# Kernel tuning notes

Hardware: AMD Instinct MI355X
Metric: run time of the kernel (lower is better)

Reference implementation:

```python
import jax, jax.numpy as jnp
import numpy as np

N_NODES = 100000
N_EDGES = 3200000
N_FEAT = 128
HIDDEN = 16
N_CLASSES = 10
N_GRAPHS = 512


def setup_inputs() -> dict:
    key = jax.random.key(0)
    ks = jax.random.split(key, 12)
    x = jax.random.normal(ks[0], (N_NODES, N_FEAT), dtype=jnp.float32)
    edge_index = jax.random.randint(ks[1], (2, N_EDGES), 0, N_NODES, dtype=jnp.int64)
    batch = jnp.sort(jax.random.randint(ks[2], (N_NODES,), 0, N_GRAPHS, dtype=jnp.int64))
    def glorot(k, fan_in, fan_out):
        s = jnp.sqrt(6.0 / (fan_in + fan_out)).astype(jnp.float32)
        return jax.random.uniform(k, (fan_in, fan_out), jnp.float32, -s, s)
    W1 = glorot(ks[3], N_FEAT, HIDDEN); b1 = jnp.zeros((HIDDEN,), jnp.float32)
    W2 = glorot(ks[4], HIDDEN, HIDDEN); b2 = jnp.zeros((HIDDEN,), jnp.float32)
    W3 = glorot(ks[5], HIDDEN, HIDDEN); b3 = jnp.zeros((HIDDEN,), jnp.float32)
    Wlin = glorot(ks[6], HIDDEN, N_CLASSES)
    blin = jnp.zeros((N_CLASSES,), jnp.float32)
    return {"x": x, "edge_index": edge_index, "batch": batch,
            "W1": W1, "b1": b1, "W2": W2, "b2": b2, "W3": W3, "b3": b3,
            "Wlin": Wlin, "blin": blin}


def _gcn_conv(x, W, b, src, dst, norm, n):
    # h = X W ; out[dst] += norm * h[src] ; + bias
    h = x @ W
    out = jax.ops.segment_sum(h[src] * norm[:, None], dst, num_segments=n)
    return out + b


def reference(x, edge_index, batch, W1, b1, W2, b2, W3, b3, Wlin, blin):
    n = x.shape[0]
    loop = jnp.arange(n, dtype=edge_index.dtype)
    src = jnp.concatenate([edge_index[0], loop])  # add self-loops (PyG GCNConv default)
    dst = jnp.concatenate([edge_index[1], loop])
    # symmetric degree normalization: deg over destination (incl. self-loops)
    deg = jax.ops.segment_sum(jnp.ones_like(dst, dtype=x.dtype), dst, num_segments=n)
    dinv = jnp.where(deg > 0, jax.lax.rsqrt(jnp.maximum(deg, 1.0)), 0.0)
    norm = dinv[src] * dinv[dst]  # [E+N]

    h = jax.nn.relu(_gcn_conv(x, W1, b1, src, dst, norm, n))
    h = jax.nn.relu(_gcn_conv(h, W2, b2, src, dst, norm, n))
    h = _gcn_conv(h, W3, b3, src, dst, norm, n)
    # global add pool over graphs
    pooled = jax.ops.segment_sum(h, batch, num_segments=N_GRAPHS)  # [G, hidden]
    # dropout p=0.5 is identity in eval mode
    return pooled @ Wlin + blin
```

## Files before the change

### kernel.cpp

```cpp
#include <hip/hip_runtime.h>
#include <hip/hip_fp16.h>

#define N_NODES   100000
#define N_EDGES   3200000
#define N_FEAT    128
#define HIDDEN    16
#define N_CLASSES 10
#define N_GRAPHS  512
#define NPB       256
#define NBUCKET   391
#define SLACK     9216
#define EPT       16


__global__ void cursor_init_kernel(int* __restrict__ cur) {
    int i = blockIdx.x * 256 + threadIdx.x;
    if (i < NBUCKET) cur[i] = i * SLACK;
}

__global__ void partition_kernel(const int* __restrict__ src, const int* __restrict__ dst,
                                 int* __restrict__ cur, unsigned* __restrict__ part) {
    __shared__ int cnt[NBUCKET];
    __shared__ int rk[NBUCKET];
    __shared__ int base[NBUCKET];
    int tid = threadIdx.x;
    for (int i = tid; i < NBUCKET; i += 256) { cnt[i] = 0; rk[i] = 0; }
    __syncthreads();
    int s0 = blockIdx.x * (256 * EPT);
#pragma unroll
    for (int i = 0; i < EPT; ++i) {
        int e = s0 + i * 256 + tid;
        if (e < N_EDGES) atomicAdd(&cnt[dst[e] >> 8], 1);
    }
    __syncthreads();
    for (int i = tid; i < NBUCKET; i += 256) {
        int c = cnt[i];
        base[i] = c ? atomicAdd(&cur[i], c) : 0;
    }
    __syncthreads();
#pragma unroll
    for (int i = 0; i < EPT; ++i) {
        int e = s0 + i * 256 + tid;
        if (e < N_EDGES) {
            int d = dst[e];
            int b = d >> 8;
            int r = atomicAdd(&rk[b], 1);
            part[base[b] + r] = (unsigned)src[e] | ((unsigned)(d & 255) << 17);
        }
    }
}

__global__ void build_csr_kernel(const unsigned* __restrict__ part, const int* __restrict__ cur,
                                 int* __restrict__ rp_beg, int* __restrict__ rp_end,
                                 float* __restrict__ dinv, int* __restrict__ csr) {
    __shared__ int ncnt[256];
    __shared__ int s[256];
    int b   = blockIdx.x;
    int tid = threadIdx.x;
    int beg = b * SLACK, end = cur[b];
    ncnt[tid] = 0;
    __syncthreads();
    for (int j = beg + tid; j < end; j += 256)
        atomicAdd(&ncnt[(part[j] >> 17) & 255], 1);
    __syncthreads();
    int deg = ncnt[tid];
    s[tid] = deg;
    __syncthreads();
    for (int off = 1; off < 256; off <<= 1) {
        int t = (tid >= off) ? s[tid - off] : 0;
        __syncthreads();
        s[tid] += t;
        __syncthreads();
    }
    int excl = s[tid] - deg;
    int node = b * 256 + tid;
    if (node < N_NODES) {
        rp_beg[node] = beg + excl;
        rp_end[node] = beg + excl + deg;
        dinv[node]   = rsqrtf((float)(deg + 1));
    }
    ncnt[tid] = beg + excl;
    __syncthreads();
    for (int j = beg + tid; j < end; j += 256) {
        unsigned r = part[j];
        int v = (r >> 17) & 255;
        int slot = atomicAdd(&ncnt[v], 1);
        csr[slot] = (int)(r & 0x1FFFFu);
    }
}


__device__ __forceinline__ void pack_store_row(__half* dstp, int v, const float* o) {
    int4 w0, w1;
    __half2 q;
    q = __floats2half2_rn(o[0],  o[1]);  w0.x = *(int*)&q;
    q = __floats2half2_rn(o[2],  o[3]);  w0.y = *(int*)&q;
    q = __floats2half2_rn(o[4],  o[5]);  w0.z = *(int*)&q;
    q = __floats2half2_rn(o[6],  o[7]);  w0.w = *(int*)&q;
    q = __floats2half2_rn(o[8],  o[9]);  w1.x = *(int*)&q;
    q = __floats2half2_rn(o[10], o[11]); w1.y = *(int*)&q;
    q = __floats2half2_rn(o[12], o[13]); w1.z = *(int*)&q;
    q = __floats2half2_rn(o[14], o[15]); w1.w = *(int*)&q;
    ((int4*)dstp)[v * 2]     = w0;
    ((int4*)dstp)[v * 2 + 1] = w1;
}

__global__ void transform_x_kernel(const float* __restrict__ x, const float* __restrict__ W,
                                   const float* __restrict__ dinv, __half* __restrict__ g) {
    __shared__ float Wl[N_FEAT * HIDDEN];
    int tid = threadIdx.x;
    for (int i = tid; i < N_FEAT * HIDDEN; i += 256) Wl[i] = W[i];
    __syncthreads();
    int v = blockIdx.x * 256 + tid;
    if (v >= N_NODES) return;
    float acc[HIDDEN];
#pragma unroll
    for (int f = 0; f < HIDDEN; ++f) acc[f] = 0.f;
    const float4* xr = (const float4*)(x + (size_t)v * N_FEAT);
#pragma unroll 4
    for (int k4 = 0; k4 < N_FEAT / 4; ++k4) {
        float4 xv = xr[k4];
        const float* wr = &Wl[k4 * 4 * HIDDEN];
#pragma unroll
        for (int f = 0; f < HIDDEN; ++f)
            acc[f] += xv.x * wr[f] + xv.y * wr[HIDDEN + f] +
                      xv.z * wr[2 * HIDDEN + f] + xv.w * wr[3 * HIDDEN + f];
    }
    float di = dinv[v];
#pragma unroll
    for (int f = 0; f < HIDDEN; ++f) acc[f] *= di;
    pack_store_row(g, v, acc);
}

__global__ void transform_h_kernel(const __half* __restrict__ h, const float* __restrict__ W,
                                   const float* __restrict__ dinv, __half* __restrict__ g) {
    __shared__ float Wl[HIDDEN * HIDDEN];
    int tid = threadIdx.x;
    if (tid < HIDDEN * HIDDEN) Wl[tid] = W[tid];
    __syncthreads();
    int v = blockIdx.x * 256 + tid;
    if (v >= N_NODES) return;
    int4 r0 = ((const int4*)h)[v * 2];
    int4 r1 = ((const int4*)h)[v * 2 + 1];
    float hv[HIDDEN];
    {
        const int rr[8] = {r0.x, r0.y, r0.z, r0.w, r1.x, r1.y, r1.z, r1.w};
#pragma unroll
        for (int q = 0; q < 8; ++q) {
            __half2 p = *(const __half2*)&rr[q];
            float2 f2 = __half22float2(p);
            hv[q * 2] = f2.x; hv[q * 2 + 1] = f2.y;
        }
    }
    float acc[HIDDEN];
#pragma unroll
    for (int f = 0; f < HIDDEN; ++f) acc[f] = 0.f;
#pragma unroll
    for (int k = 0; k < HIDDEN; ++k) {
        float hk = hv[k];
#pragma unroll
        for (int f = 0; f < HIDDEN; ++f) acc[f] += hk * Wl[k * HIDDEN + f];
    }
    float di = dinv[v];
#pragma unroll
    for (int f = 0; f < HIDDEN; ++f) acc[f] *= di;
    pack_store_row(g, v, acc);
}

__global__ void aggregate_kernel(const __half* __restrict__ g, const int* __restrict__ rp_beg,
                                 const int* __restrict__ rp_end, const int* __restrict__ csr,
                                 const float* __restrict__ dinv, const float* __restrict__ bias,
                                 __half* __restrict__ hout, int do_relu) {
    int tid  = threadIdx.x;
    int wave = tid >> 6;
    int l    = tid & 63;
    int c  = l >> 4;
    int vl = (l & 15) >> 1;
    int hh = l & 1;
    int v = blockIdx.x * 32 + wave * 8 + vl;
    if (v >= N_NODES) return;
    int beg = rp_beg[v];
    int deg = rp_end[v] - beg;
    int j0 = beg + ((deg * c) >> 2);
    int j1 = beg + ((deg * (c + 1)) >> 2);
    const int4* g4 = (const int4*)g;
    float a0 = 0.f, a1 = 0.f, a2 = 0.f, a3 = 0.f, a4 = 0.f, a5 = 0.f, a6 = 0.f, a7 = 0.f;
#pragma unroll 4
    for (int j = j0; j < j1; ++j) {
        int s = csr[j];
        int4 r = g4[s * 2 + hh];
        float2 f0 = __half22float2(*(const __half2*)&r.x);
        float2 f1 = __half22float2(*(const __half2*)&r.y);
        float2 f2 = __half22float2(*(const __half2*)&r.z);
        float2 f3 = __half22float2(*(const __half2*)&r.w);
        a0 += f0.x; a1 += f0.y; a2 += f1.x; a3 += f1.y;
        a4 += f2.x; a5 += f2.y; a6 += f3.x; a7 += f3.y;
    }
    a0 += __shfl_xor(a0, 16); a1 += __shfl_xor(a1, 16);
    a2 += __shfl_xor(a2, 16); a3 += __shfl_xor(a3, 16);
    a4 += __shfl_xor(a4, 16); a5 += __shfl_xor(a5, 16);
    a6 += __shfl_xor(a6, 16); a7 += __shfl_xor(a7, 16);
    a0 += __shfl_xor(a0, 32); a1 += __shfl_xor(a1, 32);
    a2 += __shfl_xor(a2, 32); a3 += __shfl_xor(a3, 32);
    a4 += __shfl_xor(a4, 32); a5 += __shfl_xor(a5, 32);
    a6 += __shfl_xor(a6, 32); a7 += __shfl_xor(a7, 32);
    if (c == 0) {
        int4 r = g4[v * 2 + hh];
        float2 s0 = __half22float2(*(const __half2*)&r.x);
        float2 s1 = __half22float2(*(const __half2*)&r.y);
        float2 s2 = __half22float2(*(const __half2*)&r.z);
        float2 s3 = __half22float2(*(const __half2*)&r.w);
        float di = dinv[v];
        const float4* bp = (const float4*)bias;
        float4 bA = bp[hh * 2];
        float4 bB = bp[hh * 2 + 1];
        float o0 = di * (a0 + s0.x) + bA.x;
        float o1 = di * (a1 + s0.y) + bA.y;
        float o2 = di * (a2 + s1.x) + bA.z;
        float o3 = di * (a3 + s1.y) + bA.w;
        float o4 = di * (a4 + s2.x) + bB.x;
        float o5 = di * (a5 + s2.y) + bB.y;
        float o6 = di * (a6 + s3.x) + bB.z;
        float o7 = di * (a7 + s3.y) + bB.w;
        if (do_relu) {
            o0 = fmaxf(o0, 0.f); o1 = fmaxf(o1, 0.f); o2 = fmaxf(o2, 0.f); o3 = fmaxf(o3, 0.f);
            o4 = fmaxf(o4, 0.f); o5 = fmaxf(o5, 0.f); o6 = fmaxf(o6, 0.f); o7 = fmaxf(o7, 0.f);
        }
        int4 w;
        __half2 q;
        q = __floats2half2_rn(o0, o1); w.x = *(int*)&q;
        q = __floats2half2_rn(o2, o3); w.y = *(int*)&q;
        q = __floats2half2_rn(o4, o5); w.z = *(int*)&q;
        q = __floats2half2_rn(o6, o7); w.w = *(int*)&q;
        ((int4*)hout)[v * 2 + hh] = w;
    }
}


__global__ void pool_head_kernel(const __half* __restrict__ h, const int* __restrict__ batch,
                                 const float* __restrict__ Wlin, const float* __restrict__ blin,
                                 float* __restrict__ out) {
    __shared__ float red[256];
    __shared__ int bounds[2];
    int g   = blockIdx.x;
    int tid = threadIdx.x;
    if (tid < 2) {
        int target = g + tid;
        int lo = 0, hi = N_NODES;
        while (lo < hi) {
            int mid = (lo + hi) >> 1;
            if (batch[mid] < target) lo = mid + 1; else hi = mid;
        }
        bounds[tid] = lo;
    }
    __syncthreads();
    int start = bounds[0], end = bounds[1];
    int f = tid & 15, r = tid >> 4;
    float acc = 0.f;
    for (int v = start + r; v < end; v += 16)
        acc += __half2float(h[v * HIDDEN + f]);
    red[tid] = acc;
    __syncthreads();
    for (int off = 128; off >= 16; off >>= 1) {
        if (tid < off) red[tid] += red[tid + off];
        __syncthreads();
    }
    if (tid < N_CLASSES) {
        float s = blin[tid];
#pragma unroll
        for (int fe = 0; fe < HIDDEN; ++fe) s += red[fe] * Wlin[fe * N_CLASSES + tid];
        out[g * N_CLASSES + tid] = s;
    }
}


extern "C" void kernel_launch(void* const* d_in, const int* in_sizes, int n_in,
                              void* d_out, int out_size, void* d_ws, size_t ws_size,
                              hipStream_t stream) {
    const float* x     = (const float*)d_in[0];
    const int*   ei    = (const int*)d_in[1];
    const int*   src   = ei;
    const int*   dst   = ei + N_EDGES;
    const int*   batch = (const int*)d_in[2];
    const float* W1 = (const float*)d_in[3];
    const float* b1 = (const float*)d_in[4];
    const float* W2 = (const float*)d_in[5];
    const float* b2 = (const float*)d_in[6];
    const float* W3 = (const float*)d_in[7];
    const float* b3 = (const float*)d_in[8];
    const float* Wlin = (const float*)d_in[9];
    const float* blin = (const float*)d_in[10];
    float* out = (float*)d_out;

    char* w = (char*)d_ws;
    auto alloc = [&](size_t bytes) -> char* {
        char* p = w;
        w += (bytes + 255) & ~(size_t)255;
        return p;
    };
    int*    cur    = (int*)alloc((size_t)NBUCKET * 4);
    int*    rp_beg = (int*)alloc((size_t)N_NODES * 4);
    int*    rp_end = (int*)alloc((size_t)N_NODES * 4);
    float*  dinv   = (float*)alloc((size_t)N_NODES * 4);
    __half* g      = (__half*)alloc((size_t)N_NODES * HIDDEN * 2);
    __half* hA     = (__half*)alloc((size_t)N_NODES * HIDDEN * 2);
    __half* hB     = (__half*)alloc((size_t)N_NODES * HIDDEN * 2);
    unsigned* part = (unsigned*)alloc((size_t)NBUCKET * SLACK * 4);
    int*    csr    = (int*)alloc((size_t)NBUCKET * SLACK * 4);

    int nbn = (N_NODES + 255) / 256;
    int ab  = (N_NODES + 31) / 32;
    int pb  = (N_EDGES + 256 * EPT - 1) / (256 * EPT);

    cursor_init_kernel<<<(NBUCKET + 255) / 256, 256, 0, stream>>>(cur);
    partition_kernel<<<pb, 256, 0, stream>>>(src, dst, cur, part);
    build_csr_kernel<<<NBUCKET, 256, 0, stream>>>(part, cur, rp_beg, rp_end, dinv, csr);

    transform_x_kernel<<<nbn, 256, 0, stream>>>(x, W1, dinv, g);
    aggregate_kernel<<<ab, 256, 0, stream>>>(g, rp_beg, rp_end, csr, dinv, b1, hA, 1);
    transform_h_kernel<<<nbn, 256, 0, stream>>>(hA, W2, dinv, g);
    aggregate_kernel<<<ab, 256, 0, stream>>>(g, rp_beg, rp_end, csr, dinv, b2, hB, 1);
    transform_h_kernel<<<nbn, 256, 0, stream>>>(hB, W3, dinv, g);
    aggregate_kernel<<<ab, 256, 0, stream>>>(g, rp_beg, rp_end, csr, dinv, b3, hA, 0);

    pool_head_kernel<<<N_GRAPHS, 256, 0, stream>>>(hA, batch, Wlin, blin, out);
}
```

Before: 290.2 us.

## Stage partitioned edges in shared memory for coalesced padded bucket writes; widen aggregation split

The partition kernel now bucket-sorts each 8192-edge chunk into shared memory and then writes each bucket's run contiguously to global memory, padded to 16 entries with sentinel values. Previously every edge was scattered to global memory individually. build_csr skips the sentinels, and the CSR array gets its own slack region. Separately, the aggregation kernel splits each node's edge list across 8 lane groups instead of 4, handling 4 nodes per wave, which raises parallelism per node at the cost of an extra shuffle stage and twice as many blocks.

```diff
diff --git a/kernel.cpp b/kernel.cpp
--- a/kernel.cpp
+++ b/kernel.cpp
@@ -9,44 +9,73 @@
 #define N_GRAPHS  512
 #define NPB       256
 #define NBUCKET   391
-#define SLACK     9216
-#define EPT       16
+#define EPB       8192
+#define PBLK      ((N_EDGES + EPB - 1) / EPB)
+#define PSLACK    12288
+#define CSLACK    9216
 
 
 __global__ void cursor_init_kernel(int* __restrict__ cur) {
     int i = blockIdx.x * 256 + threadIdx.x;
-    if (i < NBUCKET) cur[i] = i * SLACK;
-}
-
-__global__ void partition_kernel(const int* __restrict__ src, const int* __restrict__ dst,
-                                 int* __restrict__ cur, unsigned* __restrict__ part) {
+    if (i < NBUCKET) cur[i] = i * PSLACK;
+}
+
+__global__ __launch_bounds__(512) void partition_kernel(const int* __restrict__ src,
+                                                        const int* __restrict__ dst,
+                                                        int* __restrict__ cur,
+                                                        unsigned* __restrict__ part) {
     __shared__ int cnt[NBUCKET];
+    __shared__ int lbase[NBUCKET];
     __shared__ int rk[NBUCKET];
-    __shared__ int base[NBUCKET];
-    int tid = threadIdx.x;
-    for (int i = tid; i < NBUCKET; i += 256) { cnt[i] = 0; rk[i] = 0; }
-    __syncthreads();
-    int s0 = blockIdx.x * (256 * EPT);
-#pragma unroll
-    for (int i = 0; i < EPT; ++i) {
-        int e = s0 + i * 256 + tid;
+    __shared__ int gbase[NBUCKET];
+    __shared__ int s[512];
+    __shared__ unsigned sorted[EPB];
+    int tid = threadIdx.x;
+    for (int i = tid; i < NBUCKET; i += 512) cnt[i] = 0;
+    __syncthreads();
+    int s0 = blockIdx.x * EPB;
+#pragma unroll
+    for (int i = 0; i < EPB / 512; ++i) {
+        int e = s0 + i * 512 + tid;
         if (e < N_EDGES) atomicAdd(&cnt[dst[e] >> 8], 1);
     }
     __syncthreads();
-    for (int i = tid; i < NBUCKET; i += 256) {
-        int c = cnt[i];
-        base[i] = c ? atomicAdd(&cur[i], c) : 0;
-    }
-    __syncthreads();
-#pragma unroll
-    for (int i = 0; i < EPT; ++i) {
-        int e = s0 + i * 256 + tid;
+    int v = (tid < NBUCKET) ? cnt[tid] : 0;
+    s[tid] = v;
+    __syncthreads();
+    for (int off = 1; off < 512; off <<= 1) {
+        int t = (tid >= off) ? s[tid - off] : 0;
+        __syncthreads();
+        s[tid] += t;
+        __syncthreads();
+    }
+    if (tid < NBUCKET) {
+        int lb = s[tid] - v;
+        lbase[tid] = lb;
+        rk[tid]    = lb;
+        int cpad = (v + 15) & ~15;
+        gbase[tid] = cpad ? atomicAdd(&cur[tid], cpad) : 0;
+    }
+    __syncthreads();
+#pragma unroll
+    for (int i = 0; i < EPB / 512; ++i) {
+        int e = s0 + i * 512 + tid;
         if (e < N_EDGES) {
             int d = dst[e];
             int b = d >> 8;
             int r = atomicAdd(&rk[b], 1);
-            part[base[b] + r] = (unsigned)src[e] | ((unsigned)(d & 255) << 17);
-        }
+            sorted[r] = (unsigned)src[e] | ((unsigned)(d & 255) << 17);
+        }
+    }
+    __syncthreads();
+    int wave = tid >> 6, lane = tid & 63;
+    for (int b = wave; b < NBUCKET; b += 8) {
+        int c = cnt[b];
+        if (!c) continue;
+        int cpad = (c + 15) & ~15;
+        int lb = lbase[b], gb = gbase[b];
+        for (int j = lane; j < cpad; j += 64)
+            part[gb + j] = (j < c) ? sorted[lb + j] : 0xFFFFFFFFu;
     }
 }
 
@@ -57,11 +86,13 @@
     __shared__ int s[256];
     int b   = blockIdx.x;
     int tid = threadIdx.x;
-    int beg = b * SLACK, end = cur[b];
+    int beg = b * PSLACK, end = cur[b];
     ncnt[tid] = 0;
     __syncthreads();
-    for (int j = beg + tid; j < end; j += 256)
-        atomicAdd(&ncnt[(part[j] >> 17) & 255], 1);
+    for (int j = beg + tid; j < end; j += 256) {
+        unsigned r = part[j];
+        if (r != 0xFFFFFFFFu) atomicAdd(&ncnt[(r >> 17) & 255], 1);
+    }
     __syncthreads();
     int deg = ncnt[tid];
     s[tid] = deg;
@@ -74,18 +105,21 @@
     }
     int excl = s[tid] - deg;
     int node = b * 256 + tid;
+    int cbeg = b * CSLACK;
     if (node < N_NODES) {
-        rp_beg[node] = beg + excl;
-        rp_end[node] = beg + excl + deg;
+        rp_beg[node] = cbeg + excl;
+        rp_end[node] = cbeg + excl + deg;
         dinv[node]   = rsqrtf((float)(deg + 1));
     }
-    ncnt[tid] = beg + excl;
+    ncnt[tid] = cbeg + excl;
     __syncthreads();
     for (int j = beg + tid; j < end; j += 256) {
         unsigned r = part[j];
-        int v = (r >> 17) & 255;
-        int slot = atomicAdd(&ncnt[v], 1);
-        csr[slot] = (int)(r & 0x1FFFFu);
+        if (r != 0xFFFFFFFFu) {
+            int v = (r >> 17) & 255;
+            int slot = atomicAdd(&ncnt[v], 1);
+            csr[slot] = (int)(r & 0x1FFFFu);
+        }
     }
 }
 
@@ -174,15 +208,15 @@
     int tid  = threadIdx.x;
     int wave = tid >> 6;
     int l    = tid & 63;
-    int c  = l >> 4;
-    int vl = (l & 15) >> 1;
+    int c  = l >> 3;
+    int vl = (l >> 1) & 3;
     int hh = l & 1;
-    int v = blockIdx.x * 32 + wave * 8 + vl;
+    int v = blockIdx.x * 16 + wave * 4 + vl;
     if (v >= N_NODES) return;
     int beg = rp_beg[v];
     int deg = rp_end[v] - beg;
-    int j0 = beg + ((deg * c) >> 2);
-    int j1 = beg + ((deg * (c + 1)) >> 2);
+    int j0 = beg + ((deg * c) >> 3);
+    int j1 = beg + ((deg * (c + 1)) >> 3);
     const int4* g4 = (const int4*)g;
     float a0 = 0.f, a1 = 0.f, a2 = 0.f, a3 = 0.f, a4 = 0.f, a5 = 0.f, a6 = 0.f, a7 = 0.f;
 #pragma unroll 4
@@ -196,6 +230,10 @@
         a0 += f0.x; a1 += f0.y; a2 += f1.x; a3 += f1.y;
         a4 += f2.x; a5 += f2.y; a6 += f3.x; a7 += f3.y;
     }
+    a0 += __shfl_xor(a0, 8);  a1 += __shfl_xor(a1, 8);
+    a2 += __shfl_xor(a2, 8);  a3 += __shfl_xor(a3, 8);
+    a4 += __shfl_xor(a4, 8);  a5 += __shfl_xor(a5, 8);
+    a6 += __shfl_xor(a6, 8);  a7 += __shfl_xor(a7, 8);
     a0 += __shfl_xor(a0, 16); a1 += __shfl_xor(a1, 16);
     a2 += __shfl_xor(a2, 16); a3 += __shfl_xor(a3, 16);
     a4 += __shfl_xor(a4, 16); a5 += __shfl_xor(a5, 16);
@@ -305,15 +343,14 @@
     __half* g      = (__half*)alloc((size_t)N_NODES * HIDDEN * 2);
     __half* hA     = (__half*)alloc((size_t)N_NODES * HIDDEN * 2);
     __half* hB     = (__half*)alloc((size_t)N_NODES * HIDDEN * 2);
-    unsigned* part = (unsigned*)alloc((size_t)NBUCKET * SLACK * 4);
-    int*    csr    = (int*)alloc((size_t)NBUCKET * SLACK * 4);
+    unsigned* part = (unsigned*)alloc((size_t)NBUCKET * PSLACK * 4);
+    int*    csr    = (int*)alloc((size_t)NBUCKET * CSLACK * 4);
 
     int nbn = (N_NODES + 255) / 256;
-    int ab  = (N_NODES + 31) / 32;
-    int pb  = (N_EDGES + 256 * EPT - 1) / (256 * EPT);
+    int ab  = (N_NODES + 15) / 16;
 
     cursor_init_kernel<<<(NBUCKET + 255) / 256, 256, 0, stream>>>(cur);
-    partition_kernel<<<pb, 256, 0, stream>>>(src, dst, cur, part);
+    partition_kernel<<<PBLK, 512, 0, stream>>>(src, dst, cur, part);
     build_csr_kernel<<<NBUCKET, 256, 0, stream>>>(part, cur, rp_beg, rp_end, dinv, csr);
 
     transform_x_kernel<<<nbn, 256, 0, stream>>>(x, W1, dinv, g);
```

New measurement: 289.2 us. About the same (-0.4%).
